# Optimization experiments

Measured on AMD Instinct MI355X. Metric: run time of the kernel, lower is better.

The kernel has to match this reference:

```python
import jax, jax.numpy as jnp
import numpy as np

N_NODES = 20000
N_GRAPH = 256
NODE_DIM = 128
MULS = (128, 64, 32)       # node irreps: 128x0e + 64x1o + 32x2e
HC = 32                    # hidden channels per irrep
HIDDEN_DIM = 64
N_PATH = 9                 # feasible uuw paths into 0e+1e+2e
W_NUMEL = N_PATH * HC * HC # 9216


def _tables():
    # real Clebsch-Gordan tensors built from cartesian tensor algebra,
    # normalized so that sum(C**2) = 2*l_out + 1 (component normalization)
    eps = np.zeros((3, 3, 3))
    eps[0, 1, 2] = eps[1, 2, 0] = eps[2, 0, 1] = 1.0
    eps[0, 2, 1] = eps[2, 1, 0] = eps[1, 0, 2] = -1.0
    s2, s6 = 1 / np.sqrt(2), 1 / np.sqrt(6)
    Q2 = np.zeros((5, 3, 3))  # orthonormal basis of traceless symmetric 3x3
    Q2[0, 0, 1] = Q2[0, 1, 0] = s2          # xy
    Q2[1, 1, 2] = Q2[1, 2, 1] = s2          # yz
    Q2[2, 0, 0] = Q2[2, 1, 1] = -s6; Q2[2, 2, 2] = 2 * s6  # z2
    Q2[3, 0, 2] = Q2[3, 2, 0] = s2          # xz
    Q2[4, 0, 0] = s2; Q2[4, 1, 1] = -s2     # x2-y2

    def nrm(C, l3):
        return C * np.sqrt((2 * l3 + 1) / (C ** 2).sum())

    C000 = np.ones((1, 1, 1))
    C022 = np.eye(5)[None, :, :]
    C110 = np.eye(3).reshape(3, 3, 1) / np.sqrt(3)
    C111 = eps / np.sqrt(2)
    C112 = np.transpose(Q2, (1, 2, 0))
    C202 = np.eye(5)[:, None, :]
    C220 = np.eye(5).reshape(5, 5, 1) / np.sqrt(5)
    M = np.einsum('iab,jdb->ijad', Q2, Q2)  # [5,5,3,3]
    C221 = nrm(np.einsum('cad,ijad->ijc', eps, M), 1)
    S = 0.5 * (M + np.transpose(M, (0, 1, 3, 2)))
    S = S - np.trace(S, axis1=2, axis2=3)[..., None, None] * np.eye(3) / 3.0
    C222 = nrm(np.einsum('kad,ijad->ijk', Q2, S), 2)
    # sph2cart change of basis: 9 spherical comps (0e+1e+2e) -> 3x3 cartesian
    Qc = np.zeros((3, 3, 9))
    Qc[:, :, 0] = np.eye(3) / np.sqrt(3)        # isotropic part
    Qc[:, :, 1:4] = eps / np.sqrt(2)            # antisymmetric part
    Qc[:, :, 4:9] = np.transpose(Q2, (1, 2, 0)) # symmetric traceless part
    return [C000, C022, C110, C111, C112, C202, C220, C221, C222], Qc

_CGS, _QC = _tables()


def setup_inputs() -> dict:
    key = jax.random.key(0)
    ks = jax.random.split(key, 12)
    f32 = jnp.float32
    d_sph = MULS[0] + 3 * MULS[1] + 5 * MULS[2]  # 480
    return {
        'x_scalar': jax.random.normal(ks[0], (N_NODES, NODE_DIM), f32),
        'x_spherical': jax.random.normal(ks[1], (N_NODES, d_sph), f32),
        'batch': jnp.sort(jax.random.randint(ks[2], (N_NODES,), 0, N_GRAPH)),
        'W0e': jax.random.normal(ks[3], (MULS[0], HC), f32),
        'W1o': jax.random.normal(ks[4], (MULS[1], HC), f32),
        'W2e': jax.random.normal(ks[5], (MULS[2], HC), f32),
        'Wm1': jax.random.normal(ks[6], (NODE_DIM, HIDDEN_DIM), f32) / np.sqrt(NODE_DIM),
        'bm1': jnp.zeros((HIDDEN_DIM,), f32),
        'Wm2': jax.random.normal(ks[7], (HIDDEN_DIM, W_NUMEL), f32) / np.sqrt(HIDDEN_DIM),
        'bm2': jnp.zeros((W_NUMEL,), f32),
        'P0': jax.random.normal(ks[8], (3 * HC,), f32),
        'P1': jax.random.normal(ks[9], (2 * HC,), f32),
        'P2': jax.random.normal(ks[10], (4 * HC,), f32),
    }


def reference(x_scalar, x_spherical, batch, W0e, W1o, W2e, Wm1, bm1, Wm2, bm2, P0, P1, P2):
    n = x_scalar.shape[0]
    m0, m1, m2 = MULS
    # split node features into irrep blocks
    x0 = x_spherical[:, :m0, None]                        # [N,128,1] 0e
    x1 = x_spherical[:, m0:m0 + 3 * m1].reshape(n, m1, 3) # [N,64,3]  1o
    x2 = x_spherical[:, m0 + 3 * m1:].reshape(n, m2, 5)   # [N,32,5]  2e
    # pre_lin: per-irrep channel mixing (e3nn-style 1/sqrt(fan_in))
    h = [jnp.einsum('num,uv->nvm', x, W) / np.sqrt(W.shape[0])
         for x, W in ((x0, W0e), (x1, W1o), (x2, W2e))]   # each [N,32,2l+1]
    # per-node tensor-product weights from scalar features
    w = (jax.nn.silu(x_scalar @ Wm1 + bm1) @ Wm2 + bm2).reshape(n, N_PATH, HC, HC)
    # uuw tensor product, path order matches _CGS
    paths = ((0, 0), (0, 2), (1, 1), (1, 1), (1, 1), (2, 0), (2, 2), (2, 2), (2, 2))
    inv_u = 1.0 / np.sqrt(HC)
    outs = []
    for k, (i, j) in enumerate(paths):
        C = jnp.asarray(_CGS[k], x_scalar.dtype)
        outs.append(jnp.einsum('pqr,nup,nuq,nuw->nwr', C, h[i], h[j], w[:, k]) * inv_u)
    # post_lin: combine paths of each output l into a single channel
    y0 = jnp.einsum('num,u->nm', jnp.concatenate([outs[0], outs[2], outs[6]], 1), P0) / np.sqrt(3 * HC)
    y1 = jnp.einsum('num,u->nm', jnp.concatenate([outs[3], outs[7]], 1), P1) / np.sqrt(2 * HC)
    y2 = jnp.einsum('num,u->nm', jnp.concatenate([outs[1], outs[4], outs[5], outs[8]], 1), P2) / np.sqrt(4 * HC)
    sph = jnp.concatenate([y0, y1, y2], axis=1)           # [N,9]
    cart = jnp.einsum('abi,ni->nab', jnp.asarray(_QC, sph.dtype), sph)  # [N,3,3]
    red = jax.ops.segment_sum(cart, batch, num_segments=N_GRAPH)        # [B,3,3]
    # if_trace is False (if_iso=False): roll every non-batch dim by 1
    return jnp.roll(jnp.roll(red, 1, axis=1), 1, axis=2)
```

## Files before the change

### kernel.cpp

```cpp
#include <hip/hip_runtime.h>
#include <math.h>

#define OFF_W2P 0
#define OFF_B2P 14336
#define OFF_V   14560
#define WS_FLOATS 4494560

#define SC_Y0 0.0180421959121758f
#define SC_Y2 0.015625f
#define S2f 0.70710678118654752f
#define S6f 0.40824829046386302f
#define TWOS2f 1.41421356237309505f
#define TWOS6f 0.81649658092772603f
#define ISQRT3 0.57735026918962576f
#define ISQRT5 0.44721359549995794f
#define H0SC 0.08838834764831845f
#define H1SC 0.125f
#define H2SC 0.17677669529663689f

__device__ __constant__ int KARR[7] = {0, 1, 2, 4, 5, 6, 8};

__global__ __launch_bounds__(256) void prep_kernel(
    const float* __restrict__ Wm2, const float* __restrict__ bm2,
    const float* __restrict__ P0, const float* __restrict__ P2,
    float* __restrict__ ws, float* __restrict__ out) {
  int j = blockIdx.x * 256 + threadIdx.x;
  if (j < 2304) out[j] = 0.f;

  if (j < 14336) {
    int s = j >> 11; int rem = j & 2047; int c = rem >> 5; int u = rem & 31;
    int k = KARR[s];
    const float* P;
    float sc;
    switch (s) {
      case 0: P = P0;      sc = SC_Y0; break;
      case 1: P = P2;      sc = SC_Y2; break;
      case 2: P = P0 + 32; sc = SC_Y0; break;
      case 3: P = P2 + 32; sc = SC_Y2; break;
      case 4: P = P2 + 64; sc = SC_Y2; break;
      case 5: P = P0 + 64; sc = SC_Y0; break;
      default: P = P2 + 96; sc = SC_Y2; break;
    }
    const float4* w4 = (const float4*)(Wm2 + c * 9216 + k * 1024 + u * 32);
    const float4* p4 = (const float4*)P;
    float acc = 0.f;
#pragma unroll
    for (int q = 0; q < 8; ++q) {
      float4 a = w4[q], b = p4[q];
      acc += a.x * b.x + a.y * b.y + a.z * b.z + a.w * b.w;
    }
    ws[OFF_W2P + c * 224 + s * 32 + u] = acc * sc;
  } else if (j < 14560) {
    int i = j - 14336; int s = i >> 5; int u = i & 31; int k = KARR[s];
    const float* P;
    float sc;
    switch (s) {
      case 0: P = P0;      sc = SC_Y0; break;
      case 1: P = P2;      sc = SC_Y2; break;
      case 2: P = P0 + 32; sc = SC_Y0; break;
      case 3: P = P2 + 32; sc = SC_Y2; break;
      case 4: P = P2 + 64; sc = SC_Y2; break;
      case 5: P = P0 + 64; sc = SC_Y0; break;
      default: P = P2 + 96; sc = SC_Y2; break;
    }
    const float* b = bm2 + k * 1024 + u * 32;
    float acc = 0.f;
#pragma unroll
    for (int w = 0; w < 32; ++w) acc += b[w] * P[w];
    ws[OFF_B2P + s * 32 + u] = acc * sc;
  }
}

__global__ __launch_bounds__(256) void kv_kernel(
    const float* __restrict__ xs_g, const float* __restrict__ Wm1,
    const float* __restrict__ bm1, float* __restrict__ ws) {
  __shared__ __align__(16) float xs[16][132];
  __shared__ float hiT[64][19];
  const int tid = threadIdx.x;
  const int n0 = blockIdx.x * 16;

  for (int idx = tid; idx < 512; idx += 256) {
    const int row = idx >> 5, c4 = idx & 31;
    *(float4*)&xs[row][c4 * 4] = *(const float4*)(xs_g + (n0 + row) * 128 + c4 * 4);
  }
  __syncthreads();

  {
    const int n = tid >> 4, c0 = (tid & 15) * 4;
    float acc[4] = {0.f, 0.f, 0.f, 0.f};
#pragma unroll 4
    for (int mq = 0; mq < 32; ++mq) {
      const float4 xv = *(float4*)&xs[n][mq * 4];
      const float xa[4] = {xv.x, xv.y, xv.z, xv.w};
#pragma unroll
      for (int r = 0; r < 4; ++r) {
        const float4 w = *(const float4*)(Wm1 + (mq * 4 + r) * 64 + c0);
        acc[0] += xa[r] * w.x; acc[1] += xa[r] * w.y;
        acc[2] += xa[r] * w.z; acc[3] += xa[r] * w.w;
      }
    }
    const float4 bb = *(const float4*)(bm1 + c0);
    const float bv[4] = {bb.x, bb.y, bb.z, bb.w};
#pragma unroll
    for (int jj = 0; jj < 4; ++jj) {
      float z = acc[jj] + bv[jj];
      hiT[c0 + jj][n] = z / (1.f + __expf(-z));
    }
  }
  __syncthreads();

  if (tid < 224) {
    const int og = tid >> 3, ng = tid & 7;
    const int o0 = og * 8, n = ng * 2;
    const float4 blo = *(const float4*)(ws + OFF_B2P + o0);
    const float4 bhi = *(const float4*)(ws + OFF_B2P + o0 + 4);
    float acc[2][8];
#pragma unroll
    for (int i = 0; i < 2; ++i) {
      acc[i][0] = blo.x; acc[i][1] = blo.y; acc[i][2] = blo.z; acc[i][3] = blo.w;
      acc[i][4] = bhi.x; acc[i][5] = bhi.y; acc[i][6] = bhi.z; acc[i][7] = bhi.w;
    }
#pragma unroll 2
    for (int c = 0; c < 64; ++c) {
      const float h0v = hiT[c][n], h1v = hiT[c][n + 1];
      const float4 wlo = *(const float4*)(ws + OFF_W2P + c * 224 + o0);
      const float4 whi = *(const float4*)(ws + OFF_W2P + c * 224 + o0 + 4);
      const float wv[8] = {wlo.x, wlo.y, wlo.z, wlo.w, whi.x, whi.y, whi.z, whi.w};
#pragma unroll
      for (int jj = 0; jj < 8; ++jj) {
        acc[0][jj] += h0v * wv[jj];
        acc[1][jj] += h1v * wv[jj];
      }
    }
#pragma unroll
    for (int i = 0; i < 2; ++i) {
      const int n_g = n0 + n + i;
      float4 a = {acc[i][0], acc[i][1], acc[i][2], acc[i][3]};
      float4 b = {acc[i][4], acc[i][5], acc[i][6], acc[i][7]};
      *(float4*)(ws + OFF_V + n_g * 224 + o0) = a;
      *(float4*)(ws + OFF_V + n_g * 224 + o0 + 4) = b;
    }
  }
}

__global__ __launch_bounds__(256) void khd_kernel(
    const float* __restrict__ xsph, const int* __restrict__ batch,
    const float* __restrict__ W0e, const float* __restrict__ W1o,
    const float* __restrict__ W2e,
    const float* __restrict__ ws, float* __restrict__ out, const float norm2) {
  __shared__ __align__(16) char smem[26080];
  float (*xp)[484]    = (float (*)[484])smem;
  float (*h0s)[36]    = (float (*)[36])(smem + 15488);
  float (*h1s)[3][36] = (float (*)[3][36])(smem + 16640);
  float (*h2s)[5][36] = (float (*)[5][36])(smem + 20096);
  float (*sphs)[6]    = (float (*)[6])(smem + 25856);
  int* batch_s        = (int*)(smem + 26048);

  const int tid = threadIdx.x;
  const int n0 = blockIdx.x * 8;

  const int nl = tid >> 5, u = tid & 31;
  const float* Vg = ws + OFF_V + (size_t)(n0 + nl) * 224 + u;
  const float v0 = Vg[0],   v1 = Vg[32],  v2 = Vg[64],  v3 = Vg[96];
  const float v4 = Vg[128], v5 = Vg[160], v6 = Vg[192];

  if (tid < 8) batch_s[tid] = batch[n0 + tid];

  for (int idx = tid; idx < 960; idx += 256) {
    const int row = idx / 120, c4 = idx % 120;
    *(float4*)&xp[row][c4 * 4] =
        *(const float4*)(xsph + (size_t)(n0 + row) * 480 + c4 * 4);
  }
  __syncthreads();

  if (tid < 64) {
    const int n = tid & 7, u0 = ((tid >> 3) & 7) * 4;
    float acc[2][4] = {{0.f}};
#pragma unroll 2
    for (int mq = 0; mq < 16; ++mq) {
      const float4 a0 = *(float4*)&xp[n][128 + mq * 12];
      const float4 a1 = *(float4*)&xp[n][128 + mq * 12 + 4];
      const float4 a2 = *(float4*)&xp[n][128 + mq * 12 + 8];
      const float xa[12] = {a0.x, a0.y, a0.z, a0.w, a1.x, a1.y, a1.z, a1.w,
                            a2.x, a2.y, a2.z, a2.w};
#pragma unroll
      for (int mm = 0; mm < 4; ++mm) {
        const float4 w = *(const float4*)(W1o + (mq * 4 + mm) * 32 + u0);
        const float wv[4] = {w.x, w.y, w.z, w.w};
#pragma unroll
        for (int j = 0; j < 2; ++j) {
          const float xr = xa[mm * 3 + j];
#pragma unroll
          for (int jj = 0; jj < 4; ++jj) acc[j][jj] += xr * wv[jj];
        }
      }
    }
#pragma unroll
    for (int j = 0; j < 2; ++j) {
      float4 a = {acc[j][0] * H1SC, acc[j][1] * H1SC, acc[j][2] * H1SC, acc[j][3] * H1SC};
      *(float4*)&h1s[n][j][u0] = a;
    }
  } else if (tid < 128) {
    const int t = tid - 64;
    const int n = t & 7, u0 = ((t >> 3) & 7) * 4;
    float acc[4][4] = {{0.f}};
#pragma unroll 2
    for (int mq = 0; mq < 8; ++mq) {
      const float4 a0 = *(float4*)&xp[n][320 + mq * 20];
      const float4 a1 = *(float4*)&xp[n][320 + mq * 20 + 4];
      const float4 a2 = *(float4*)&xp[n][320 + mq * 20 + 8];
      const float4 a3 = *(float4*)&xp[n][320 + mq * 20 + 12];
      const float4 a4 = *(float4*)&xp[n][320 + mq * 20 + 16];
      const float xa[20] = {a0.x, a0.y, a0.z, a0.w, a1.x, a1.y, a1.z, a1.w,
                            a2.x, a2.y, a2.z, a2.w, a3.x, a3.y, a3.z, a3.w,
                            a4.x, a4.y, a4.z, a4.w};
#pragma unroll
      for (int mm = 0; mm < 4; ++mm) {
        const float4 w = *(const float4*)(W2e + (mq * 4 + mm) * 32 + u0);
        const float wv[4] = {w.x, w.y, w.z, w.w};
#pragma unroll
        for (int j = 1; j < 5; ++j) {
          const float xr = xa[mm * 5 + j];
#pragma unroll
          for (int jj = 0; jj < 4; ++jj) acc[j - 1][jj] += xr * wv[jj];
        }
      }
    }
#pragma unroll
    for (int j = 1; j < 5; ++j) {
      float4 a = {acc[j - 1][0] * H2SC, acc[j - 1][1] * H2SC,
                  acc[j - 1][2] * H2SC, acc[j - 1][3] * H2SC};
      *(float4*)&h2s[n][j][u0] = a;
    }
  } else if (tid < 192) {
    const int t = tid - 128;
    const int n = t & 7, u0 = ((t >> 3) & 7) * 4;
    float acc[4] = {0.f, 0.f, 0.f, 0.f};
#pragma unroll 4
    for (int mq = 0; mq < 32; ++mq) {
      const float4 xv = *(float4*)&xp[n][mq * 4];
      const float xa[4] = {xv.x, xv.y, xv.z, xv.w};
#pragma unroll
      for (int r = 0; r < 4; ++r) {
        const float4 w = *(const float4*)(W0e + (mq * 4 + r) * 32 + u0);
        acc[0] += xa[r] * w.x; acc[1] += xa[r] * w.y;
        acc[2] += xa[r] * w.z; acc[3] += xa[r] * w.w;
      }
    }
    float4 a = {acc[0] * H0SC, acc[1] * H0SC, acc[2] * H0SC, acc[3] * H0SC};
    *(float4*)&h0s[n][u0] = a;
  } else {
    const int t = tid - 192;
    const int n = t & 7, u0 = ((t >> 3) & 7) * 4;
    float acc1[4] = {0.f, 0.f, 0.f, 0.f};
#pragma unroll 2
    for (int mq = 0; mq < 16; ++mq) {
      const float4 a0 = *(float4*)&xp[n][128 + mq * 12];
      const float4 a1 = *(float4*)&xp[n][128 + mq * 12 + 4];
      const float4 a2 = *(float4*)&xp[n][128 + mq * 12 + 8];
      const float xa[12] = {a0.x, a0.y, a0.z, a0.w, a1.x, a1.y, a1.z, a1.w,
                            a2.x, a2.y, a2.z, a2.w};
#pragma unroll
      for (int mm = 0; mm < 4; ++mm) {
        const float4 w = *(const float4*)(W1o + (mq * 4 + mm) * 32 + u0);
        const float xr = xa[mm * 3 + 2];
        acc1[0] += xr * w.x; acc1[1] += xr * w.y;
        acc1[2] += xr * w.z; acc1[3] += xr * w.w;
      }
    }
    {
      float4 a = {acc1[0] * H1SC, acc1[1] * H1SC, acc1[2] * H1SC, acc1[3] * H1SC};
      *(float4*)&h1s[n][2][u0] = a;
    }
    float acc2[4] = {0.f, 0.f, 0.f, 0.f};
#pragma unroll 2
    for (int mq = 0; mq < 8; ++mq) {
      const float4 a0 = *(float4*)&xp[n][320 + mq * 20];
      const float4 a1 = *(float4*)&xp[n][320 + mq * 20 + 4];
      const float4 a2 = *(float4*)&xp[n][320 + mq * 20 + 8];
      const float4 a3 = *(float4*)&xp[n][320 + mq * 20 + 12];
      const float4 a4 = *(float4*)&xp[n][320 + mq * 20 + 16];
      const float xa[20] = {a0.x, a0.y, a0.z, a0.w, a1.x, a1.y, a1.z, a1.w,
                            a2.x, a2.y, a2.z, a2.w, a3.x, a3.y, a3.z, a3.w,
                            a4.x, a4.y, a4.z, a4.w};
#pragma unroll
      for (int mm = 0; mm < 4; ++mm) {
        const float4 w = *(const float4*)(W2e + (mq * 4 + mm) * 32 + u0);
        const float xr = xa[mm * 5 + 0];
        acc2[0] += xr * w.x; acc2[1] += xr * w.y;
        acc2[2] += xr * w.z; acc2[3] += xr * w.w;
      }
    }
    {
      float4 a = {acc2[0] * H2SC, acc2[1] * H2SC, acc2[2] * H2SC, acc2[3] * H2SC};
      *(float4*)&h2s[n][0][u0] = a;
    }
  }
  __syncthreads();

  {
    const float h0 = h0s[nl][u];
    const float h1a = h1s[nl][0][u], h1b = h1s[nl][1][u], h1c = h1s[nl][2][u];
    float h2v[5];
#pragma unroll
    for (int j = 0; j < 5; ++j) h2v[j] = h2s[nl][j][u];

    const float d11 = h1a * h1a + h1b * h1b + h1c * h1c;
    const float d22 = h2v[0] * h2v[0] + h2v[1] * h2v[1] + h2v[2] * h2v[2] +
                      h2v[3] * h2v[3] + h2v[4] * h2v[4];
    float y0 = v0 * h0 * h0 + v2 * d11 * ISQRT3 + v5 * d22 * ISQRT5;

    const float o00 = h1a * h1a, o01 = h1a * h1b, o02 = h1a * h1c;
    const float o11 = h1b * h1b, o12 = h1b * h1c, o22 = h1c * h1c;
    const float t40 = TWOS2f * o01, t41 = TWOS2f * o12;
    const float t42 = S6f * (2.f * o22 - o00 - o11);
    const float t43 = TWOS2f * o02, t44 = S2f * (o00 - o11);

    const float A00 = -S6f * h2v[2] + S2f * h2v[4];
    const float A01 = S2f * h2v[0];
    const float A02 = S2f * h2v[3];
    const float A11 = -S6f * h2v[2] - S2f * h2v[4];
    const float A12 = S2f * h2v[1];
    const float A22 = TWOS6f * h2v[2];
    const float B00 = A00 * A00 + A01 * A01 + A02 * A02;
    const float B01 = A00 * A01 + A01 * A11 + A02 * A12;
    const float B02 = A00 * A02 + A01 * A12 + A02 * A22;
    const float B11 = A01 * A01 + A11 * A11 + A12 * A12;
    const float B12 = A01 * A02 + A11 * A12 + A12 * A22;
    const float B22 = A02 * A02 + A12 * A12 + A22 * A22;
    const float t80 = TWOS2f * B01, t81 = TWOS2f * B12;
    const float t82 = S6f * (2.f * B22 - B00 - B11);
    const float t83 = TWOS2f * B02, t84 = S2f * (B00 - B11);

    const float w15 = (v1 + v4) * h0;
    const float v6n = v6 * norm2;
    float y2r[5];
    y2r[0] = w15 * h2v[0] + v3 * t40 + v6n * t80;
    y2r[1] = w15 * h2v[1] + v3 * t41 + v6n * t81;
    y2r[2] = w15 * h2v[2] + v3 * t42 + v6n * t82;
    y2r[3] = w15 * h2v[3] + v3 * t43 + v6n * t83;
    y2r[4] = w15 * h2v[4] + v3 * t44 + v6n * t84;

#pragma unroll
    for (int off = 16; off > 0; off >>= 1) {
      y0 += __shfl_xor(y0, off, 32);
#pragma unroll
      for (int r = 0; r < 5; ++r) y2r[r] += __shfl_xor(y2r[r], off, 32);
    }
    if (u == 0) {
      sphs[nl][0] = y0;
#pragma unroll
      for (int r = 0; r < 5; ++r) sphs[nl][1 + r] = y2r[r];
    }
  }
  __syncthreads();

  if (tid < 9) {
    const float QW[9][6] = {
        {ISQRT3, 0.f, 0.f, -S6f, 0.f, S2f},
        {0.f, S2f, 0.f, 0.f, 0.f, 0.f},
        {0.f, 0.f, 0.f, 0.f, S2f, 0.f},
        {0.f, S2f, 0.f, 0.f, 0.f, 0.f},
        {ISQRT3, 0.f, 0.f, -S6f, 0.f, -S2f},
        {0.f, 0.f, S2f, 0.f, 0.f, 0.f},
        {0.f, 0.f, 0.f, 0.f, S2f, 0.f},
        {0.f, 0.f, S2f, 0.f, 0.f, 0.f},
        {ISQRT3, 0.f, 0.f, TWOS6f, 0.f, 0.f}};
    const int a = tid / 3, b = tid % 3;
    const int rolled = ((a + 1) % 3) * 3 + ((b + 1) % 3);
    const float c0 = QW[tid][0], c1 = QW[tid][1], c2 = QW[tid][2];
    const float c3 = QW[tid][3], c4 = QW[tid][4], c5 = QW[tid][5];
    int cur_g = batch_s[0];
    float acc = 0.f;
#pragma unroll
    for (int q = 0; q < 8; ++q) {
      const int g = batch_s[q];
      const float val = c0 * sphs[q][0] + c1 * sphs[q][1] + c2 * sphs[q][2] +
                        c3 * sphs[q][3] + c4 * sphs[q][4] + c5 * sphs[q][5];
      if (g != cur_g) {
        atomicAdd(out + cur_g * 9 + rolled, acc);
        acc = 0.f;
        cur_g = g;
      }
      acc += val;
    }
    atomicAdd(out + cur_g * 9 + rolled, acc);
  }
}

extern "C" void kernel_launch(void* const* d_in, const int* in_sizes, int n_in,
                              void* d_out, int out_size, void* d_ws, size_t ws_size,
                              hipStream_t stream) {
  const float* x_scalar = (const float*)d_in[0];
  const float* x_sph    = (const float*)d_in[1];
  const int*   batch    = (const int*)d_in[2];
  const float* W0e      = (const float*)d_in[3];
  const float* W1o      = (const float*)d_in[4];
  const float* W2e      = (const float*)d_in[5];
  const float* Wm1      = (const float*)d_in[6];
  const float* bm1      = (const float*)d_in[7];
  const float* Wm2      = (const float*)d_in[8];
  const float* bm2      = (const float*)d_in[9];
  const float* P0       = (const float*)d_in[10];
  const float* P2       = (const float*)d_in[12];
  float* ws  = (float*)d_ws;
  float* out = (float*)d_out;

  if (ws_size < (size_t)WS_FLOATS * sizeof(float)) return;

  double Q2[5][3][3] = {};
  const double s2d = 0.70710678118654752440, s6d = 0.40824829046386301637;
  Q2[0][0][1] = Q2[0][1][0] = s2d;
  Q2[1][1][2] = Q2[1][2][1] = s2d;
  Q2[2][0][0] = Q2[2][1][1] = -s6d; Q2[2][2][2] = 2.0 * s6d;
  Q2[3][0][2] = Q2[3][2][0] = s2d;
  Q2[4][0][0] = s2d; Q2[4][1][1] = -s2d;
  double ss = 0.0;
  for (int i = 0; i < 5; ++i)
    for (int jj = 0; jj < 5; ++jj) {
      double S[3][3];
      for (int a = 0; a < 3; ++a)
        for (int d = 0; d < 3; ++d) {
          double m1 = 0, m2 = 0;
          for (int b = 0; b < 3; ++b) {
            m1 += Q2[i][a][b] * Q2[jj][d][b];
            m2 += Q2[i][d][b] * Q2[jj][a][b];
          }
          S[a][d] = 0.5 * (m1 + m2);
        }
      double tr = (S[0][0] + S[1][1] + S[2][2]) / 3.0;
      S[0][0] -= tr; S[1][1] -= tr; S[2][2] -= tr;
      for (int kk = 0; kk < 5; ++kk) {
        double cc = 0;
        for (int a = 0; a < 3; ++a)
          for (int d = 0; d < 3; ++d) cc += Q2[kk][a][d] * S[a][d];
        ss += cc * cc;
      }
    }
  const float norm2 = (float)sqrt(5.0 / ss);

  prep_kernel<<<57, 256, 0, stream>>>(Wm2, bm2, P0, P2, ws, out);
  kv_kernel<<<1250, 256, 0, stream>>>(x_scalar, Wm1, bm1, ws);
  khd_kernel<<<2500, 256, 0, stream>>>(x_sph, batch, W0e, W1o, W2e, ws, out, norm2);
}
```

Baseline: 173.2 us.

## Enlarge per-block node tiles and register-block both kernels for weight reuse

kv_kernel now handles 32 nodes per block with 4x4 and 8x8 register tiles in its two GEMM stages, so each global weight load is reused across more nodes. khd_kernel handles 16 nodes per block and reuses each loaded projection weight across two node halves. The aim is to cut redundant weight reads and per-block overhead. In exchange, block counts are halved, more threads sit idle in kv_kernel (only 128 and 112 active), shared memory doubles and register pressure rises, all of which may lower occupancy.

```diff
diff --git a/kernel.cpp b/kernel.cpp
--- a/kernel.cpp
+++ b/kernel.cpp
@@ -74,67 +74,78 @@
 __global__ __launch_bounds__(256) void kv_kernel(
     const float* __restrict__ xs_g, const float* __restrict__ Wm1,
     const float* __restrict__ bm1, float* __restrict__ ws) {
-  __shared__ __align__(16) float xs[16][132];
-  __shared__ float hiT[64][19];
+  __shared__ __align__(16) float xs[32][132];
+  __shared__ __align__(16) float hiT[64][36];
   const int tid = threadIdx.x;
-  const int n0 = blockIdx.x * 16;
-
-  for (int idx = tid; idx < 512; idx += 256) {
+  const int n0 = blockIdx.x * 32;
+
+  for (int idx = tid; idx < 1024; idx += 256) {
     const int row = idx >> 5, c4 = idx & 31;
     *(float4*)&xs[row][c4 * 4] = *(const float4*)(xs_g + (n0 + row) * 128 + c4 * 4);
   }
   __syncthreads();
 
-  {
-    const int n = tid >> 4, c0 = (tid & 15) * 4;
-    float acc[4] = {0.f, 0.f, 0.f, 0.f};
-#pragma unroll 4
+  if (tid < 128) {
+    const int cg = tid & 15, ng = tid >> 4;
+    const int c0 = cg * 4, nl = ng * 4;
+    float acc[4][4] = {{0.f}};
+#pragma unroll 2
     for (int mq = 0; mq < 32; ++mq) {
-      const float4 xv = *(float4*)&xs[n][mq * 4];
-      const float xa[4] = {xv.x, xv.y, xv.z, xv.w};
+      float4 xv[4], wv[4];
+#pragma unroll
+      for (int i = 0; i < 4; ++i) xv[i] = *(float4*)&xs[nl + i][mq * 4];
+#pragma unroll
+      for (int r = 0; r < 4; ++r) wv[r] = *(const float4*)(Wm1 + (mq * 4 + r) * 64 + c0);
 #pragma unroll
       for (int r = 0; r < 4; ++r) {
-        const float4 w = *(const float4*)(Wm1 + (mq * 4 + r) * 64 + c0);
-        acc[0] += xa[r] * w.x; acc[1] += xa[r] * w.y;
-        acc[2] += xa[r] * w.z; acc[3] += xa[r] * w.w;
+        const float4 w = wv[r];
+#pragma unroll
+        for (int i = 0; i < 4; ++i) {
+          const float xr = (r == 0) ? xv[i].x : (r == 1) ? xv[i].y : (r == 2) ? xv[i].z : xv[i].w;
+          acc[i][0] += xr * w.x; acc[i][1] += xr * w.y;
+          acc[i][2] += xr * w.z; acc[i][3] += xr * w.w;
+        }
       }
     }
     const float4 bb = *(const float4*)(bm1 + c0);
     const float bv[4] = {bb.x, bb.y, bb.z, bb.w};
 #pragma unroll
-    for (int jj = 0; jj < 4; ++jj) {
-      float z = acc[jj] + bv[jj];
-      hiT[c0 + jj][n] = z / (1.f + __expf(-z));
-    }
+    for (int i = 0; i < 4; ++i)
+#pragma unroll
+      for (int jj = 0; jj < 4; ++jj) {
+        float z = acc[i][jj] + bv[jj];
+        hiT[c0 + jj][nl + i] = z / (1.f + __expf(-z));
+      }
   }
   __syncthreads();
 
-  if (tid < 224) {
-    const int og = tid >> 3, ng = tid & 7;
-    const int o0 = og * 8, n = ng * 2;
+  if (tid < 112) {
+    const int og = tid >> 2, ng = tid & 3;
+    const int o0 = og * 8, nl = ng * 8;
     const float4 blo = *(const float4*)(ws + OFF_B2P + o0);
     const float4 bhi = *(const float4*)(ws + OFF_B2P + o0 + 4);
-    float acc[2][8];
-#pragma unroll
-    for (int i = 0; i < 2; ++i) {
+    float acc[8][8];
+#pragma unroll
+    for (int i = 0; i < 8; ++i) {
       acc[i][0] = blo.x; acc[i][1] = blo.y; acc[i][2] = blo.z; acc[i][3] = blo.w;
       acc[i][4] = bhi.x; acc[i][5] = bhi.y; acc[i][6] = bhi.z; acc[i][7] = bhi.w;
     }
 #pragma unroll 2
     for (int c = 0; c < 64; ++c) {
-      const float h0v = hiT[c][n], h1v = hiT[c][n + 1];
+      const float4 ha = *(float4*)&hiT[c][nl];
+      const float4 hb = *(float4*)&hiT[c][nl + 4];
       const float4 wlo = *(const float4*)(ws + OFF_W2P + c * 224 + o0);
       const float4 whi = *(const float4*)(ws + OFF_W2P + c * 224 + o0 + 4);
+      const float hv[8] = {ha.x, ha.y, ha.z, ha.w, hb.x, hb.y, hb.z, hb.w};
       const float wv[8] = {wlo.x, wlo.y, wlo.z, wlo.w, whi.x, whi.y, whi.z, whi.w};
 #pragma unroll
-      for (int jj = 0; jj < 8; ++jj) {
-        acc[0][jj] += h0v * wv[jj];
-        acc[1][jj] += h1v * wv[jj];
-      }
-    }
-#pragma unroll
-    for (int i = 0; i < 2; ++i) {
-      const int n_g = n0 + n + i;
+      for (int i = 0; i < 8; ++i)
+#pragma unroll
+        for (int jj = 0; jj < 8; ++jj) acc[i][jj] += hv[i] * wv[jj];
+    }
+#pragma unroll
+    for (int i = 0; i < 8; ++i) {
+      const int n_g = n0 + nl + i;
       float4 a = {acc[i][0], acc[i][1], acc[i][2], acc[i][3]};
       float4 b = {acc[i][4], acc[i][5], acc[i][6], acc[i][7]};
       *(float4*)(ws + OFF_V + n_g * 224 + o0) = a;
@@ -148,25 +159,31 @@
     const float* __restrict__ W0e, const float* __restrict__ W1o,
     const float* __restrict__ W2e,
     const float* __restrict__ ws, float* __restrict__ out, const float norm2) {
-  __shared__ __align__(16) char smem[26080];
+  __shared__ __align__(16) char smem[52160];
   float (*xp)[484]    = (float (*)[484])smem;
-  float (*h0s)[36]    = (float (*)[36])(smem + 15488);
-  float (*h1s)[3][36] = (float (*)[3][36])(smem + 16640);
-  float (*h2s)[5][36] = (float (*)[5][36])(smem + 20096);
-  float (*sphs)[6]    = (float (*)[6])(smem + 25856);
-  int* batch_s        = (int*)(smem + 26048);
+  float (*h0s)[36]    = (float (*)[36])(smem + 30976);
+  float (*h1s)[3][36] = (float (*)[3][36])(smem + 33280);
+  float (*h2s)[5][36] = (float (*)[5][36])(smem + 40192);
+  float (*sphs)[6]    = (float (*)[6])(smem + 51712);
+  int* batch_s        = (int*)(smem + 52096);
 
   const int tid = threadIdx.x;
-  const int n0 = blockIdx.x * 8;
-
-  const int nl = tid >> 5, u = tid & 31;
-  const float* Vg = ws + OFF_V + (size_t)(n0 + nl) * 224 + u;
-  const float v0 = Vg[0],   v1 = Vg[32],  v2 = Vg[64],  v3 = Vg[96];
-  const float v4 = Vg[128], v5 = Vg[160], v6 = Vg[192];
-
-  if (tid < 8) batch_s[tid] = batch[n0 + tid];
-
-  for (int idx = tid; idx < 960; idx += 256) {
+  const int n0 = blockIdx.x * 16;
+
+  const int nl8 = tid >> 5, u = tid & 31;
+  float vreg[2][7];
+  {
+    const float* Vg0 = ws + OFF_V + (size_t)(n0 + nl8) * 224 + u;
+    const float* Vg1 = Vg0 + 8 * 224;
+#pragma unroll
+    for (int s = 0; s < 7; ++s) {
+      vreg[0][s] = Vg0[s * 32];
+      vreg[1][s] = Vg1[s * 32];
+    }
+  }
+  if (tid < 16) batch_s[tid] = batch[n0 + tid];
+
+  for (int idx = tid; idx < 1920; idx += 256) {
     const int row = idx / 120, c4 = idx % 120;
     *(float4*)&xp[row][c4 * 4] =
         *(const float4*)(xsph + (size_t)(n0 + row) * 480 + c4 * 4);
@@ -174,136 +191,196 @@
   __syncthreads();
 
   if (tid < 64) {
-    const int n = tid & 7, u0 = ((tid >> 3) & 7) * 4;
+    const int n8 = tid & 7, u0 = ((tid >> 3) & 7) * 4;
+    float acc[2][2][4] = {{{0.f}}};
+#pragma unroll 2
+    for (int mq = 0; mq < 16; ++mq) {
+      float wv[4][4];
+#pragma unroll
+      for (int mm = 0; mm < 4; ++mm) {
+        const float4 w = *(const float4*)(W1o + (mq * 4 + mm) * 32 + u0);
+        wv[mm][0] = w.x; wv[mm][1] = w.y; wv[mm][2] = w.z; wv[mm][3] = w.w;
+      }
+#pragma unroll
+      for (int half = 0; half < 2; ++half) {
+        const int n = half * 8 + n8;
+        const float4 a0 = *(float4*)&xp[n][128 + mq * 12];
+        const float4 a1 = *(float4*)&xp[n][128 + mq * 12 + 4];
+        const float4 a2 = *(float4*)&xp[n][128 + mq * 12 + 8];
+        const float xa[12] = {a0.x, a0.y, a0.z, a0.w, a1.x, a1.y, a1.z, a1.w,
+                              a2.x, a2.y, a2.z, a2.w};
+#pragma unroll
+        for (int mm = 0; mm < 4; ++mm)
+#pragma unroll
+          for (int j = 0; j < 2; ++j) {
+            const float xr = xa[mm * 3 + j];
+#pragma unroll
+            for (int jj = 0; jj < 4; ++jj) acc[half][j][jj] += xr * wv[mm][jj];
+          }
+      }
+    }
+#pragma unroll
+    for (int half = 0; half < 2; ++half)
+#pragma unroll
+      for (int j = 0; j < 2; ++j) {
+        float4 a = {acc[half][j][0] * H1SC, acc[half][j][1] * H1SC,
+                    acc[half][j][2] * H1SC, acc[half][j][3] * H1SC};
+        *(float4*)&h1s[half * 8 + n8][j][u0] = a;
+      }
+  } else if (tid < 128) {
+    const int t = tid - 64;
+    const int n8 = t & 7, u0 = ((t >> 3) & 7) * 4;
+    float acc[2][4][4] = {{{0.f}}};
+#pragma unroll 1
+    for (int mq = 0; mq < 8; ++mq) {
+      float wv[4][4];
+#pragma unroll
+      for (int mm = 0; mm < 4; ++mm) {
+        const float4 w = *(const float4*)(W2e + (mq * 4 + mm) * 32 + u0);
+        wv[mm][0] = w.x; wv[mm][1] = w.y; wv[mm][2] = w.z; wv[mm][3] = w.w;
+      }
+#pragma unroll
+      for (int half = 0; half < 2; ++half) {
+        const int n = half * 8 + n8;
+        const float4 a0 = *(float4*)&xp[n][320 + mq * 20];
+        const float4 a1 = *(float4*)&xp[n][320 + mq * 20 + 4];
+        const float4 a2 = *(float4*)&xp[n][320 + mq * 20 + 8];
+        const float4 a3 = *(float4*)&xp[n][320 + mq * 20 + 12];
+        const float4 a4 = *(float4*)&xp[n][320 + mq * 20 + 16];
+        const float xa[20] = {a0.x, a0.y, a0.z, a0.w, a1.x, a1.y, a1.z, a1.w,
+                              a2.x, a2.y, a2.z, a2.w, a3.x, a3.y, a3.z, a3.w,
+                              a4.x, a4.y, a4.z, a4.w};
+#pragma unroll
+        for (int mm = 0; mm < 4; ++mm)
+#pragma unroll
+          for (int j = 1; j < 5; ++j) {
+            const float xr = xa[mm * 5 + j];
+#pragma unroll
+            for (int jj = 0; jj < 4; ++jj) acc[half][j - 1][jj] += xr * wv[mm][jj];
+          }
+      }
+    }
+#pragma unroll
+    for (int half = 0; half < 2; ++half)
+#pragma unroll
+      for (int j = 1; j < 5; ++j) {
+        float4 a = {acc[half][j - 1][0] * H2SC, acc[half][j - 1][1] * H2SC,
+                    acc[half][j - 1][2] * H2SC, acc[half][j - 1][3] * H2SC};
+        *(float4*)&h2s[half * 8 + n8][j][u0] = a;
+      }
+  } else if (tid < 192) {
+    const int t = tid - 128;
+    const int n8 = t & 7, u0 = ((t >> 3) & 7) * 4;
     float acc[2][4] = {{0.f}};
 #pragma unroll 2
+    for (int mq = 0; mq < 32; ++mq) {
+      float wv[4][4];
+#pragma unroll
+      for (int r = 0; r < 4; ++r) {
+        const float4 w = *(const float4*)(W0e + (mq * 4 + r) * 32 + u0);
+        wv[r][0] = w.x; wv[r][1] = w.y; wv[r][2] = w.z; wv[r][3] = w.w;
+      }
+#pragma unroll
+      for (int half = 0; half < 2; ++half) {
+        const int n = half * 8 + n8;
+        const float4 xv = *(float4*)&xp[n][mq * 4];
+        const float xa[4] = {xv.x, xv.y, xv.z, xv.w};
+#pragma unroll
+        for (int r = 0; r < 4; ++r) {
+          const float xr = xa[r];
+#pragma unroll
+          for (int jj = 0; jj < 4; ++jj) acc[half][jj] += xr * wv[r][jj];
+        }
+      }
+    }
+#pragma unroll
+    for (int half = 0; half < 2; ++half) {
+      float4 a = {acc[half][0] * H0SC, acc[half][1] * H0SC,
+                  acc[half][2] * H0SC, acc[half][3] * H0SC};
+      *(float4*)&h0s[half * 8 + n8][u0] = a;
+    }
+  } else {
+    const int t = tid - 192;
+    const int n8 = t & 7, u0 = ((t >> 3) & 7) * 4;
+    float acc1[2][4] = {{0.f}};
+#pragma unroll 2
     for (int mq = 0; mq < 16; ++mq) {
-      const float4 a0 = *(float4*)&xp[n][128 + mq * 12];
-      const float4 a1 = *(float4*)&xp[n][128 + mq * 12 + 4];
-      const float4 a2 = *(float4*)&xp[n][128 + mq * 12 + 8];
-      const float xa[12] = {a0.x, a0.y, a0.z, a0.w, a1.x, a1.y, a1.z, a1.w,
-                            a2.x, a2.y, a2.z, a2.w};
+      float wv[4][4];
 #pragma unroll
       for (int mm = 0; mm < 4; ++mm) {
         const float4 w = *(const float4*)(W1o + (mq * 4 + mm) * 32 + u0);
-        const float wv[4] = {w.x, w.y, w.z, w.w};
-#pragma unroll
-        for (int j = 0; j < 2; ++j) {
-          const float xr = xa[mm * 3 + j];
-#pragma unroll
-          for (int jj = 0; jj < 4; ++jj) acc[j][jj] += xr * wv[jj];
+        wv[mm][0] = w.x; wv[mm][1] = w.y; wv[mm][2] = w.z; wv[mm][3] = w.w;
+      }
+#pragma unroll
+      for (int half = 0; half < 2; ++half) {
+        const int n = half * 8 + n8;
+        const float4 a0 = *(float4*)&xp[n][128 + mq * 12];
+        const float4 a1 = *(float4*)&xp[n][128 + mq * 12 + 4];
+        const float4 a2 = *(float4*)&xp[n][128 + mq * 12 + 8];
+        const float xa[12] = {a0.x, a0.y, a0.z, a0.w, a1.x, a1.y, a1.z, a1.w,
+                              a2.x, a2.y, a2.z, a2.w};
+#pragma unroll
+        for (int mm = 0; mm < 4; ++mm) {
+          const float xr = xa[mm * 3 + 2];
+#pragma unroll
+          for (int jj = 0; jj < 4; ++jj) acc1[half][jj] += xr * wv[mm][jj];
         }
       }
     }
 #pragma unroll
-    for (int j = 0; j < 2; ++j) {
-      float4 a = {acc[j][0] * H1SC, acc[j][1] * H1SC, acc[j][2] * H1SC, acc[j][3] * H1SC};
-      *(float4*)&h1s[n][j][u0] = a;
-    }
-  } else if (tid < 128) {
-    const int t = tid - 64;
-    const int n = t & 7, u0 = ((t >> 3) & 7) * 4;
-    float acc[4][4] = {{0.f}};
-#pragma unroll 2
+    for (int half = 0; half < 2; ++half) {
+      float4 a = {acc1[half][0] * H1SC, acc1[half][1] * H1SC,
+                  acc1[half][2] * H1SC, acc1[half][3] * H1SC};
+      *(float4*)&h1s[half * 8 + n8][2][u0] = a;
+    }
+    float acc2[2][4] = {{0.f}};
+#pragma unroll 1
     for (int mq = 0; mq < 8; ++mq) {
-      const float4 a0 = *(float4*)&xp[n][320 + mq * 20];
-      const float4 a1 = *(float4*)&xp[n][320 + mq * 20 + 4];
-      const float4 a2 = *(float4*)&xp[n][320 + mq * 20 + 8];
-      const float4 a3 = *(float4*)&xp[n][320 + mq * 20 + 12];
-      const float4 a4 = *(float4*)&xp[n][320 + mq * 20 + 16];
-      const float xa[20] = {a0.x, a0.y, a0.z, a0.w, a1.x, a1.y, a1.z, a1.w,
-                            a2.x, a2.y, a2.z, a2.w, a3.x, a3.y, a3.z, a3.w,
-                            a4.x, a4.y, a4.z, a4.w};
+      float wv[4][4];
 #pragma unroll
       for (int mm = 0; mm < 4; ++mm) {
         const float4 w = *(const float4*)(W2e + (mq * 4 + mm) * 32 + u0);
-        const float wv[4] = {w.x, w.y, w.z, w.w};
-#pragma unroll
-        for (int j = 1; j < 5; ++j) {
-          const float xr = xa[mm * 5 + j];
-#pragma unroll
-          for (int jj = 0; jj < 4; ++jj) acc[j - 1][jj] += xr * wv[jj];
+        wv[mm][0] = w.x; wv[mm][1] = w.y; wv[mm][2] = w.z; wv[mm][3] = w.w;
+      }
+#pragma unroll
+      for (int half = 0; half < 2; ++half) {
+        const int n = half * 8 + n8;
+        const float4 a0 = *(float4*)&xp[n][320 + mq * 20];
+        const float4 a1 = *(float4*)&xp[n][320 + mq * 20 + 4];
+        const float4 a2 = *(float4*)&xp[n][320 + mq * 20 + 8];
+        const float4 a3 = *(float4*)&xp[n][320 + mq * 20 + 12];
+        const float4 a4 = *(float4*)&xp[n][320 + mq * 20 + 16];
+        const float xa[20] = {a0.x, a0.y, a0.z, a0.w, a1.x, a1.y, a1.z, a1.w,
+                              a2.x, a2.y, a2.z, a2.w, a3.x, a3.y, a3.z, a3.w,
+                              a4.x, a4.y, a4.z, a4.w};
+#pragma unroll
+        for (int mm = 0; mm < 4; ++mm) {
+          const float xr = xa[mm * 5 + 0];
+#pragma unroll
+          for (int jj = 0; jj < 4; ++jj) acc2[half][jj] += xr * wv[mm][jj];
         }
       }
     }
 #pragma unroll
-    for (int j = 1; j < 5; ++j) {
-      float4 a = {acc[j - 1][0] * H2SC, acc[j - 1][1] * H2SC,
-                  acc[j - 1][2] * H2SC, acc[j - 1][3] * H2SC};
-      *(float4*)&h2s[n][j][u0] = a;
-    }
-  } else if (tid < 192) {
-    const int t = tid - 128;
-    const int n = t & 7, u0 = ((t >> 3) & 7) * 4;
-    float acc[4] = {0.f, 0.f, 0.f, 0.f};
-#pragma unroll 4
-    for (int mq = 0; mq < 32; ++mq) {
-      const float4 xv = *(float4*)&xp[n][mq * 4];
-      const float xa[4] = {xv.x, xv.y, xv.z, xv.w};
-#pragma unroll
-      for (int r = 0; r < 4; ++r) {
-        const float4 w = *(const float4*)(W0e + (mq * 4 + r) * 32 + u0);
-        acc[0] += xa[r] * w.x; acc[1] += xa[r] * w.y;
-        acc[2] += xa[r] * w.z; acc[3] += xa[r] * w.w;
-      }
-    }
-    float4 a = {acc[0] * H0SC, acc[1] * H0SC, acc[2] * H0SC, acc[3] * H0SC};
-    *(float4*)&h0s[n][u0] = a;
-  } else {
-    const int t = tid - 192;
-    const int n = t & 7, u0 = ((t >> 3) & 7) * 4;
-    float acc1[4] = {0.f, 0.f, 0.f, 0.f};
+    for (int half = 0; half < 2; ++half) {
+      float4 a = {acc2[half][0] * H2SC, acc2[half][1] * H2SC,
+                  acc2[half][2] * H2SC, acc2[half][3] * H2SC};
+      *(float4*)&h2s[half * 8 + n8][0][u0] = a;
+    }
+  }
+  __syncthreads();
+
 #pragma unroll 2
-    for (int mq = 0; mq < 16; ++mq) {
-      const float4 a0 = *(float4*)&xp[n][128 + mq * 12];
-      const float4 a1 = *(float4*)&xp[n][128 + mq * 12 + 4];
-      const float4 a2 = *(float4*)&xp[n][128 + mq * 12 + 8];
-      const float xa[12] = {a0.x, a0.y, a0.z, a0.w, a1.x, a1.y, a1.z, a1.w,
-                            a2.x, a2.y, a2.z, a2.w};
-#pragma unroll
-      for (int mm = 0; mm < 4; ++mm) {
-        const float4 w = *(const float4*)(W1o + (mq * 4 + mm) * 32 + u0);
-        const float xr = xa[mm * 3 + 2];
-        acc1[0] += xr * w.x; acc1[1] += xr * w.y;
-        acc1[2] += xr * w.z; acc1[3] += xr * w.w;
-      }
-    }
-    {
-      float4 a = {acc1[0] * H1SC, acc1[1] * H1SC, acc1[2] * H1SC, acc1[3] * H1SC};
-      *(float4*)&h1s[n][2][u0] = a;
-    }
-    float acc2[4] = {0.f, 0.f, 0.f, 0.f};
-#pragma unroll 2
-    for (int mq = 0; mq < 8; ++mq) {
-      const float4 a0 = *(float4*)&xp[n][320 + mq * 20];
-      const float4 a1 = *(float4*)&xp[n][320 + mq * 20 + 4];
-      const float4 a2 = *(float4*)&xp[n][320 + mq * 20 + 8];
-      const float4 a3 = *(float4*)&xp[n][320 + mq * 20 + 12];
-      const float4 a4 = *(float4*)&xp[n][320 + mq * 20 + 16];
-      const float xa[20] = {a0.x, a0.y, a0.z, a0.w, a1.x, a1.y, a1.z, a1.w,
-                            a2.x, a2.y, a2.z, a2.w, a3.x, a3.y, a3.z, a3.w,
-                            a4.x, a4.y, a4.z, a4.w};
-#pragma unroll
-      for (int mm = 0; mm < 4; ++mm) {
-        const float4 w = *(const float4*)(W2e + (mq * 4 + mm) * 32 + u0);
-        const float xr = xa[mm * 5 + 0];
-        acc2[0] += xr * w.x; acc2[1] += xr * w.y;
-        acc2[2] += xr * w.z; acc2[3] += xr * w.w;
-      }
-    }
-    {
-      float4 a = {acc2[0] * H2SC, acc2[1] * H2SC, acc2[2] * H2SC, acc2[3] * H2SC};
-      *(float4*)&h2s[n][0][u0] = a;
-    }
-  }
-  __syncthreads();
-
-  {
-    const float h0 = h0s[nl][u];
-    const float h1a = h1s[nl][0][u], h1b = h1s[nl][1][u], h1c = h1s[nl][2][u];
+  for (int half = 0; half < 2; ++half) {
+    const int n = half * 8 + nl8;
+    const float h0 = h0s[n][u];
+    const float h1a = h1s[n][0][u], h1b = h1s[n][1][u], h1c = h1s[n][2][u];
     float h2v[5];
 #pragma unroll
-    for (int j = 0; j < 5; ++j) h2v[j] = h2s[nl][j][u];
+    for (int j = 0; j < 5; ++j) h2v[j] = h2s[n][j][u];
+    const float v0 = vreg[half][0], v1 = vreg[half][1], v2 = vreg[half][2],
+                v3 = vreg[half][3], v4 = vreg[half][4], v5 = vreg[half][5],
+                v6 = vreg[half][6];
 
     const float d11 = h1a * h1a + h1b * h1b + h1c * h1c;
     const float d22 = h2v[0] * h2v[0] + h2v[1] * h2v[1] + h2v[2] * h2v[2] +
@@ -348,9 +425,9 @@
       for (int r = 0; r < 5; ++r) y2r[r] += __shfl_xor(y2r[r], off, 32);
     }
     if (u == 0) {
-      sphs[nl][0] = y0;
-#pragma unroll
-      for (int r = 0; r < 5; ++r) sphs[nl][1 + r] = y2r[r];
+      sphs[n][0] = y0;
+#pragma unroll
+      for (int r = 0; r < 5; ++r) sphs[n][1 + r] = y2r[r];
     }
   }
   __syncthreads();
@@ -372,8 +449,8 @@
     const float c3 = QW[tid][3], c4 = QW[tid][4], c5 = QW[tid][5];
     int cur_g = batch_s[0];
     float acc = 0.f;
-#pragma unroll
-    for (int q = 0; q < 8; ++q) {
+#pragma unroll 4
+    for (int q = 0; q < 16; ++q) {
       const int g = batch_s[q];
       const float val = c0 * sphs[q][0] + c1 * sphs[q][1] + c2 * sphs[q][2] +
                         c3 * sphs[q][3] + c4 * sphs[q][4] + c5 * sphs[q][5];
@@ -440,6 +517,6 @@
   const float norm2 = (float)sqrt(5.0 / ss);
 
   prep_kernel<<<57, 256, 0, stream>>>(Wm2, bm2, P0, P2, ws, out);
-  kv_kernel<<<1250, 256, 0, stream>>>(x_scalar, Wm1, bm1, ws);
-  khd_kernel<<<2500, 256, 0, stream>>>(x_sph, batch, W0e, W1o, W2e, ws, out, norm2);
+  kv_kernel<<<625, 256, 0, stream>>>(x_scalar, Wm1, bm1, ws);
+  khd_kernel<<<1250, 256, 0, stream>>>(x_sph, batch, W0e, W1o, W2e, ws, out, norm2);
 }
```

Result: faster. 160.7 us (-7.2%).
